# Performance work log

Hardware: AMD Instinct MI355X
Metric: run time of the kernel (lower is better)

## Reference

```python
import jax, jax.numpy as jnp
import numpy as np

N, C, H, W = 4, 256, 64, 64
S = 2          # scale_factor
K = 5          # up_kernel
G = 1          # up_group
CK = 64        # compressed_channels


def conv2d(x, w, b, pad):
    out = jax.lax.conv_general_dilated(
        x, w, window_strides=(1, 1), padding=[(pad, pad), (pad, pad)],
        dimension_numbers=('NCHW', 'OIHW', 'NCHW'))
    return out + b[None, :, None, None]


def pixel_shuffle(x, r):
    n, cr, h, w = x.shape
    c = cr // (r * r)
    return x.reshape(n, c, r, r, h, w).transpose(0, 1, 4, 2, 5, 3).reshape(n, c, h * r, w * r)


def grid_sample_border(img, grid):
    # img [N,C,Hi,Wi], grid [N,Ho,Wo,2] in [-1,1] (x,y); bilinear, border pad, align_corners=True
    n, c, hi, wi = img.shape
    gx = (grid[..., 0] + 1.0) * 0.5 * (wi - 1)
    gy = (grid[..., 1] + 1.0) * 0.5 * (hi - 1)
    gx = jnp.clip(gx, 0.0, wi - 1.0)
    gy = jnp.clip(gy, 0.0, hi - 1.0)
    x0 = jnp.floor(gx).astype(jnp.int32)
    y0 = jnp.floor(gy).astype(jnp.int32)
    x1 = jnp.minimum(x0 + 1, wi - 1)
    y1 = jnp.minimum(y0 + 1, hi - 1)
    wx = (gx - x0)[..., None]
    wy = (gy - y0)[..., None]
    bidx = jnp.arange(n)[:, None, None]
    def gather(yy, xx):
        return img[bidx, :, yy, xx]  # [N,Ho,Wo,C]
    v00 = gather(y0, x0)
    v01 = gather(y0, x1)
    v10 = gather(y1, x0)
    v11 = gather(y1, x1)
    out = (v00 * (1 - wx) * (1 - wy) + v01 * wx * (1 - wy)
           + v10 * (1 - wx) * wy + v11 * wx * wy)
    return out.transpose(0, 3, 1, 2)


def carafe2(features, masks, k, g, up):
    n, c, h, w = features.shape
    cg = c // g
    k2 = k * k
    # masks [N, g*k2, h*up, w*up] -> per-pixel kernels [n,g,h,w,k2,up2]
    m = masks.reshape(n, g, k2, h, up, w, up)
    m = m.transpose(0, 1, 2, 3, 5, 4, 6).reshape(n, g, k2, h, w, up * up)
    kern = m.transpose(0, 1, 3, 4, 2, 5)            # [n,g,h,w,k2,up2]
    f = features.reshape(n, g, cg, h, w)
    p = k // 2
    fp = jnp.pad(f, ((0, 0), (0, 0), (0, 0), (p, p), (p, p)))
    patches = jnp.stack([fp[:, :, :, i:i + h, j:j + w]
                         for i in range(k) for j in range(k)], axis=-1)  # [n,g,cg,h,w,k2]
    xp = patches.transpose(0, 1, 3, 4, 2, 5)        # [n,g,h,w,cg,k2]
    out = jnp.einsum('nghwck,nghwku->nghwcu', xp, kern)  # [n,g,h,w,cg,up2]
    out = out.transpose(0, 1, 4, 2, 3, 5).reshape(n, c * up * up, h, w)
    return pixel_shuffle(out, up)


def setup_inputs() -> dict:
    key = jax.random.key(0)
    ks = jax.random.split(key, 4)
    x = jax.random.normal(ks[0], (N, C, H, W), dtype=jnp.float32)
    w_comp = jax.random.normal(ks[1], (CK, C, 1, 1), dtype=jnp.float32) * 0.05
    b_comp = jnp.zeros((CK,), dtype=jnp.float32)
    w_ker = jax.random.normal(ks[2], (G * K * K, CK, 3, 3), dtype=jnp.float32) * 0.001
    b_ker = jnp.zeros((G * K * K,), dtype=jnp.float32)
    w_off = jax.random.normal(ks[3], (G * 2 * S * S, CK, 3, 3), dtype=jnp.float32) * 0.01
    b_off = jnp.zeros((G * 2 * S * S,), dtype=jnp.float32)
    return {'x': x, 'w_comp': w_comp, 'b_comp': b_comp,
            'w_ker': w_ker, 'b_ker': b_ker, 'w_off': w_off, 'b_off': b_off}


def reference(x, w_comp, b_comp, w_ker, b_ker, w_off, b_off):
    cx = conv2d(x, w_comp, b_comp, 0)               # channel compressor (1x1)
    offset = conv2d(cx, w_off, b_off, 1)            # [N, 2*S*S, H, W]
    mask = conv2d(cx, w_ker, b_ker, 1)              # [N, G*K*K, H, W]
    # kernel_space_normalizer: softmax over the K*K kernel positions
    n, mc, h, w = mask.shape
    mask = jax.nn.softmax(mask.reshape(n, mc // (K * K), K * K, h, w), axis=2)
    mask = mask.reshape(n, mc, h, w)
    # kernel_space_expander
    off = pixel_shuffle(offset, S).transpose(0, 2, 3, 1)  # [N, H*S, W*S, 2]
    off = off * jnp.array([2.0 / (w - 1), 2.0 / (h - 1)], dtype=off.dtype)
    gh = jnp.repeat(jnp.linspace(-1.0, 1.0, h), S)  # [H*S]
    gw = jnp.repeat(jnp.linspace(-1.0, 1.0, w), S)  # [W*S]
    base = jnp.stack(jnp.broadcast_arrays(gw[None, :], gh[:, None]), axis=-1)  # [H*S, W*S, 2]
    grid = base[None] + off
    mask_ = grid_sample_border(mask, grid)          # [N, G*K*K, H*S, W*S]
    return carafe2(x, mask_, K, G, S)
```

## Files before the change

### kernel.cpp

```cpp
#include <hip/hip_runtime.h>
#include <math.h>

#define NB 4
#define C_IN 256
#define CKC 64
#define HWSZ 4096
#define K2 25
#define NOC2 40

#define WS_CX    0
#define WS_OFF   (WS_CX + NB*CKC*HWSZ)
#define WS_MASK  (WS_OFF + NB*8*HWSZ)
#define WS_WT    (WS_MASK + NB*K2*HWSZ)

#define NWT (CKC * 9 * NOC2)
#define NWC (C_IN * CKC)

#define BARRIER_LDS() do { \
    asm volatile("s_waitcnt lgkmcnt(0)" ::: "memory"); \
    __builtin_amdgcn_s_barrier(); \
  } while (0)

__global__ void k_wt(const float* __restrict__ wk, const float* __restrict__ wo,
                     const float* __restrict__ wc,
                     float* __restrict__ wT, float* __restrict__ wcT) {
  int i = blockIdx.x * 256 + threadIdx.x;
  if (i < NWT) {
    int oc = i % NOC2;
    int r = i / NOC2;
    int tap = r % 9, c = r / 9;
    float v = 0.f;
    if (oc < 8)       v = wo[(oc * CKC + c) * 9 + tap];
    else if (oc < 33) v = wk[((oc - 8) * CKC + c) * 9 + tap];
    wT[i] = v;
  } else {
    int j = i - NWT;
    if (j < NWC) {
      int c = j >> 6, ck = j & 63;
      wcT[j] = wc[ck * C_IN + c];
    }
  }
}

__global__ __launch_bounds__(1024) void k_cs(const float* __restrict__ x,
    const float* __restrict__ wcT, const float* __restrict__ bc,
    const float* __restrict__ wT, const float* __restrict__ bk, const float* __restrict__ bo,
    float* __restrict__ offb, float* __restrict__ maskb) {
  __attribute__((aligned(16))) __shared__ float s_mem[15360];
  float* s_tile = s_mem;
  float* s_res  = s_mem;

  int t = threadIdx.x;
  int n = blockIdx.y;
  int tile = blockIdx.x;
  int x0 = (tile & 3) * 16, y0 = (tile >> 2) * 4;
  const float* xn = x + (size_t)n * (C_IN * HWSZ);

  int p = t & 63;
  int w = t >> 6;
  int g = __builtin_amdgcn_readfirstlane(w & 7);
  int ch = __builtin_amdgcn_readfirstlane(w >> 3);

  int srcOff[4];
  unsigned vbits = 0, wbits = 0;
  #pragma unroll
  for (int it = 0; it < 4; it++) {
    int e = t + it * 1024;
    int c = e / 60;
    int rem = e - c * 60;
    int row = rem / 10, pr = rem - row * 10;
    int gy = y0 - 1 + row;
    int gc0 = x0 - 2 + pr * 2;
    bool wr = (e < 3840);
    bool ok = wr & ((unsigned)gy < 64u) & ((unsigned)gc0 < 63u);
    srcOff[it] = ok ? (c * HWSZ + gy * 64 + gc0) : 0;
    vbits |= (ok ? 1u : 0u) << it;
    wbits |= (wr ? 1u : 0u) << it;
  }

  int q1 = p + 60;
  int q1c = (q1 < 120) ? q1 : 119;
  int r0q = p / 20,  c0q = p - r0q * 20;
  int r1q = q1c / 20, c1q = q1c - r1q * 20;
  bool val0 = (c0q >= 1) & (c0q <= 18);
  bool val1 = (q1 < 120) & (c1q >= 1) & (c1q <= 18);
  int toff0 = r0q * 24 + c0q - 1;
  int toff1 = r1q * 24 + c1q - 1;
  float a0[8], a1[8];
  #pragma unroll
  for (int i = 0; i < 8; i++) {
    float b = (ch == 0) ? bc[g * 8 + i] : 0.f;
    a0[i] = b; a1[i] = b;
  }

  float2 rv[4];
  #pragma unroll
  for (int it = 0; it < 4; it++) rv[it] = *(const float2*)(xn + srcOff[it]);

  float* sA = s_mem;
  float* sB = s_mem + 7680;
  #pragma unroll
  for (int it = 0; it < 4; it++)
    if (wbits & (1u << it))
      *(float2*)(&sA[2 * t + it * 2048]) =
          (vbits & (1u << it)) ? rv[it] : make_float2(0.f, 0.f);
  {
    const float* xb = xn + (size_t)64 * HWSZ;
    #pragma unroll
    for (int it = 0; it < 4; it++) rv[it] = *(const float2*)(xb + srcOff[it]);
  }
  BARRIER_LDS();

  for (int k = 0; k < 4; k++) {
    if (k < 3) {
      #pragma unroll
      for (int it = 0; it < 4; it++)
        if (wbits & (1u << it))
          *(float2*)(&sB[2 * t + it * 2048]) =
              (vbits & (1u << it)) ? rv[it] : make_float2(0.f, 0.f);
    }
    if (k < 2) {
      const float* xb = xn + (size_t)(k + 2) * 64 * HWSZ;
      #pragma unroll
      for (int it = 0; it < 4; it++) rv[it] = *(const float2*)(xb + srcOff[it]);
    }
    if ((k >> 1) == ch) {
      const float* wbase = wcT + (k * 64) * 64 + g * 8;
      #pragma unroll 4
      for (int c = 0; c < 64; c++) {
        float v0 = sA[c * 120 + p];
        float v1 = sA[c * 120 + q1c];
        const float* wp = wbase + c * 64;
        #pragma unroll
        for (int i = 0; i < 8; i++) { a0[i] += v0 * wp[i]; a1[i] += v1 * wp[i]; }
      }
    }
    BARRIER_LDS();
    float* tmp = sA; sA = sB; sB = tmp;
  }

  if (ch == 1) {
    if (val0) {
      #pragma unroll
      for (int i = 0; i < 8; i++) s_tile[(g * 8 + i) * 144 + toff0] = a0[i];
    }
    if (val1) {
      #pragma unroll
      for (int i = 0; i < 8; i++) s_tile[(g * 8 + i) * 144 + toff1] = a1[i];
    }
  }
  BARRIER_LDS();
  if (ch == 0) {
    if (val0) {
      #pragma unroll
      for (int i = 0; i < 8; i++) {
        int idx = (g * 8 + i) * 144 + toff0;
        s_tile[idx] = s_tile[idx] + a0[i];
      }
    }
    if (val1) {
      #pragma unroll
      for (int i = 0; i < 8; i++) {
        int idx = (g * 8 + i) * 144 + toff1;
        s_tile[idx] = s_tile[idx] + a1[i];
      }
    }
  }
  BARRIER_LDS();

  int px = p & 15, py = p >> 4;
  float acc[5];
  #pragma unroll
  for (int j = 0; j < 5; j++) acc[j] = 0.f;
  const float* wg = wT + g * 5;
  const float* tl0 = s_tile + py * 24 + px;
  int cb = ch * 32;

#define LOADWIN(dst, cidx)                                   \
  {                                                          \
    const float* tlc = tl0 + (cidx) * 144;                   \
    _Pragma("unroll")                                        \
    for (int tap = 0; tap < 9; tap++) {                      \
      int dy = tap / 3, dx = tap % 3;                        \
      dst[tap] = tlc[dy * 24 + dx];                          \
    }                                                        \
  }
#define FMAWIN(src, cidx)                                    \
  {                                                          \
    const float* wc9 = wg + (cidx) * 9 * NOC2;               \
    _Pragma("unroll")                                        \
    for (int tap = 0; tap < 9; tap++) {                      \
      float v = src[tap];                                    \
      const float* wp = wc9 + tap * NOC2;                    \
      _Pragma("unroll")                                      \
      for (int j = 0; j < 5; j++) acc[j] += v * wp[j];       \
    }                                                        \
  }

  float wa[9], wbuf[9];
  LOADWIN(wa, cb + 0)
  LOADWIN(wbuf, cb + 1)
  #pragma unroll 1
  for (int c = 0; c < 32; c += 2) {
    FMAWIN(wa, cb + c)
    if (c + 2 < 32) LOADWIN(wa, cb + c + 2)
    FMAWIN(wbuf, cb + c + 1)
    if (c + 3 < 32) LOADWIN(wbuf, cb + c + 3)
  }
#undef LOADWIN
#undef FMAWIN

  BARRIER_LDS();
  if (ch == 0) {
    #pragma unroll
    for (int j = 0; j < 5; j++) s_res[(g * 5 + j) * 64 + p] = acc[j];
  }
  BARRIER_LDS();
  if (ch == 1) {
    #pragma unroll
    for (int j = 0; j < 5; j++) s_res[(g * 5 + j) * 64 + p] += acc[j];
  }
  BARRIER_LDS();

  int hw = (y0 + py) * 64 + x0 + px;
  if (ch == 0)
    offb[(n * 8 + g) * HWSZ + hw] = s_res[g * 64 + p] + bo[g];
  if (t < 64) {
    float m[25], mx = -1e30f;
    #pragma unroll
    for (int k = 0; k < 25; k++) { m[k] = s_res[(8 + k) * 64 + p] + bk[k]; mx = fmaxf(mx, m[k]); }
    float s = 0.f;
    #pragma unroll
    for (int k = 0; k < 25; k++) { m[k] = __expf(m[k] - mx); s += m[k]; }
    float inv = 1.f / s;
    #pragma unroll
    for (int k = 0; k < 25; k++) maskb[(n * 25 + k) * HWSZ + hw] = m[k] * inv;
  }
}

__global__ __launch_bounds__(256, 4) void k_carafe(const float* __restrict__ x,
    const float* __restrict__ offb, const float* __restrict__ maskb,
    float* __restrict__ out) {
  __attribute__((aligned(16))) __shared__ float s_patch[32 * 202];
  __attribute__((aligned(16))) __shared__ float s_kern[32 * 25 * 4];
  int t = threadIdx.x;
  int b = blockIdx.x;
  int n = b >> 8;
  int r = b & 255;
  int half = r & 1;
  int wq = (r >> 1) & 3;
  int aa = r >> 3;
  int a = aa + (aa & 16);
  int yout = (a & 15) * 8 + wq * 2 + ((a >> 5) & 1);
  int w0 = wq * 16;
  int cbase = n * C_IN + half * 128;

  int srcOff[13];
  int dstOff[13];
  unsigned vbits = 0;
  unsigned wbits = 0;
  #pragma unroll
  for (int it = 0; it < 13; it++) {
    int e = t + it * 256;
    int c = e / 100;
    int rem = e - c * 100;
    int rg = rem / 10;
    int c2 = rem - rg * 10;
    int row = (rg < 5) ? (a - 2 + rg) : (a + 9 + rg);
    int gc0 = w0 - 2 + c2 * 2;
    bool wr = (e < 3200);
    bool ok = wr & ((unsigned)row < 64u) & ((unsigned)gc0 < 64u);
    srcOff[it] = ok ? (c * HWSZ + row * 64 + gc0) : 0;
    dstOff[it] = wr ? 2 * (e + c) : 0;
    vbits |= (ok ? 1u : 0u) << it;
    wbits |= (wr ? 1u : 0u) << it;
  }

  float2 rv[13];
  {
    const float* xn = x + (size_t)cbase * HWSZ;
    #pragma unroll
    for (int it = 0; it < 13; it++) rv[it] = *(const float2*)(xn + srcOff[it]);
  }

  if (t < 128) {
    int p = t >> 2, u = t & 3;
    int hb = p >> 4, wl = p & 15;
    int h = a + hb * 16;
    int wcol = w0 + wl;
    float ox = offb[(n * 8 + u) * HWSZ + h * 64 + wcol];
    float oy = offb[(n * 8 + 4 + u) * HWSZ + h * 64 + wcol];
    float gx = fminf(fmaxf((float)wcol + ox, 0.f), 63.f);
    float gy = fminf(fmaxf((float)h + oy, 0.f), 63.f);
    float fx0 = floorf(gx), fy0 = floorf(gy);
    int x0 = (int)fx0, y0 = (int)fy0;
    float fx = gx - fx0, fy = gy - fy0;
    int x1 = min(x0 + 1, 63), y1 = min(y0 + 1, 63);
    float w11 = fx * fy;
    float w10 = fy - w11, w01 = fx - w11, w00 = 1.f - fx - fy + w11;
    const float* mb = maskb + n * (K2 * HWSZ);
    int i00 = y0 * 64 + x0, i01 = y0 * 64 + x1;
    int i10 = y1 * 64 + x0, i11 = y1 * 64 + x1;
    #pragma unroll 5
    for (int k = 0; k < 25; k++) {
      const float* mk = mb + k * HWSZ;
      float v = w00 * mk[i00] + w01 * mk[i01] + w10 * mk[i10] + w11 * mk[i11];
      s_kern[(p * 25 + k) * 4 + u] = v;
    }
  }

  int cl = t & 31, g = t >> 5;
  int hb = g >> 2, wl0 = (g & 3) * 4;
  float* s_out = s_patch;

  for (int cc = 0; cc < 4; cc++) {
    BARRIER_LDS();
    #pragma unroll
    for (int it = 0; it < 13; it++) {
      if (wbits & (1u << it)) {
        float2 v = (vbits & (1u << it)) ? rv[it] : make_float2(0.f, 0.f);
        *(float2*)(&s_patch[dstOff[it]]) = v;
      }
    }
    BARRIER_LDS();
    if (cc < 3) {
      const float* xn = x + (size_t)(cbase + (cc + 1) * 32) * HWSZ;
      #pragma unroll
      for (int it = 0; it < 13; it++) rv[it] = *(const float2*)(xn + srcOff[it]);
    }
    float acc[4][4];
    #pragma unroll
    for (int i = 0; i < 4; i++)
      acc[i][0] = acc[i][1] = acc[i][2] = acc[i][3] = 0.f;
    const float* pc = s_patch + cl * 202 + hb * 100 + wl0;
    #pragma unroll
    for (int dy = 0; dy < 5; dy++) {
      float r8[8];
      #pragma unroll
      for (int j = 0; j < 8; j++) r8[j] = pc[dy * 20 + j];
      #pragma unroll
      for (int pr = 0; pr < 4; pr++) {
        const float4* kp = (const float4*)(s_kern + (((g * 4 + pr) * 25) + dy * 5) * 4);
        #pragma unroll
        for (int dx = 0; dx < 5; dx++) {
          float f = r8[pr + dx];
          float4 k4 = kp[dx];
          acc[pr][0] += f * k4.x;
          acc[pr][1] += f * k4.y;
          acc[pr][2] += f * k4.z;
          acc[pr][3] += f * k4.w;
        }
      }
    }
    BARRIER_LDS();
    #pragma unroll
    for (int pr = 0; pr < 4; pr++) {
      int wl = wl0 + pr;
      #pragma unroll
      for (int u = 0; u < 4; u++) {
        int xo = wl * 8 + u * 2 + hb;
        s_out[cl * 130 + xo] = acc[pr][u];
      }
    }
    BARRIER_LDS();
    float* obase = out + ((size_t)(cbase + cc * 32) * 128 + yout) * 128;
    #pragma unroll
    for (int it = 0; it < 4; it++) {
      int q2 = t + it * 256;
      int rowc = q2 >> 5;
      int col4 = q2 & 31;
      const float* sp = s_out + rowc * 130 + col4 * 4;
      float4 v = make_float4(sp[0], sp[1], sp[2], sp[3]);
      *(float4*)(obase + (size_t)rowc * (128 * 128) + col4 * 4) = v;
    }
  }
}

extern "C" void kernel_launch(void* const* d_in, const int* in_sizes, int n_in,
                              void* d_out, int out_size, void* d_ws, size_t ws_size,
                              hipStream_t stream) {
  const float* x      = (const float*)d_in[0];
  const float* w_comp = (const float*)d_in[1];
  const float* b_comp = (const float*)d_in[2];
  const float* w_ker  = (const float*)d_in[3];
  const float* b_ker  = (const float*)d_in[4];
  const float* w_off  = (const float*)d_in[5];
  const float* b_off  = (const float*)d_in[6];
  float* out = (float*)d_out;
  float* ws = (float*)d_ws;
  float* offb  = ws + WS_OFF;
  float* maskb = ws + WS_MASK;
  float* wT    = ws + WS_WT;
  float* wcT   = ws + WS_CX;

  hipLaunchKernelGGL(k_wt, dim3((NWT + NWC + 255) / 256), dim3(256), 0, stream,
                     w_ker, w_off, w_comp, wT, wcT);
  hipLaunchKernelGGL(k_cs, dim3(64, 4), dim3(1024), 0, stream,
                     x, wcT, b_comp, wT, b_ker, b_off, offb, maskb);
  hipLaunchKernelGGL(k_carafe, dim3(1024), dim3(256), 0, stream, x, offb, maskb, out);
}
```

Measured before the change: 172.7 us.

## Halve k_cs spatial tile to 8x4 to double block count

Shrinks the compressor and mask/offset conv tile from 16x4 to 8x4 pixels, so the haloed input tile drops to 6x12 and each thread computes one compressed pixel instead of two. The grid doubles to 128x4 blocks, which should fill more CUs on a device with 256 CUs and cut LDS use per block. In exchange, the 3x3 halo is recomputed more often relative to useful output, and half of each wave sits idle during the 3x3 conv stage.

```diff
diff --git a/kernel.cpp b/kernel.cpp
--- a/kernel.cpp
+++ b/kernel.cpp
@@ -46,14 +46,14 @@
     const float* __restrict__ wcT, const float* __restrict__ bc,
     const float* __restrict__ wT, const float* __restrict__ bk, const float* __restrict__ bo,
     float* __restrict__ offb, float* __restrict__ maskb) {
-  __attribute__((aligned(16))) __shared__ float s_mem[15360];
+  __attribute__((aligned(16))) __shared__ float s_mem[9216];
   float* s_tile = s_mem;
   float* s_res  = s_mem;
 
   int t = threadIdx.x;
   int n = blockIdx.y;
   int tile = blockIdx.x;
-  int x0 = (tile & 3) * 16, y0 = (tile >> 2) * 4;
+  int x0 = (tile & 7) * 8, y0 = (tile >> 3) * 4;
   const float* xn = x + (size_t)n * (C_IN * HWSZ);
 
   int p = t & 63;
@@ -61,128 +61,106 @@
   int g = __builtin_amdgcn_readfirstlane(w & 7);
   int ch = __builtin_amdgcn_readfirstlane(w >> 3);
 
-  int srcOff[4];
+  int srcOff[3];
   unsigned vbits = 0, wbits = 0;
   #pragma unroll
-  for (int it = 0; it < 4; it++) {
+  for (int it = 0; it < 3; it++) {
     int e = t + it * 1024;
-    int c = e / 60;
-    int rem = e - c * 60;
-    int row = rem / 10, pr = rem - row * 10;
+    int c = e / 36;
+    int rem = e - c * 36;
+    int row = rem / 6, pr = rem - row * 6;
     int gy = y0 - 1 + row;
     int gc0 = x0 - 2 + pr * 2;
-    bool wr = (e < 3840);
+    bool wr = (e < 2304);
     bool ok = wr & ((unsigned)gy < 64u) & ((unsigned)gc0 < 63u);
     srcOff[it] = ok ? (c * HWSZ + gy * 64 + gc0) : 0;
     vbits |= (ok ? 1u : 0u) << it;
     wbits |= (wr ? 1u : 0u) << it;
   }
 
-  int q1 = p + 60;
-  int q1c = (q1 < 120) ? q1 : 119;
-  int r0q = p / 20,  c0q = p - r0q * 20;
-  int r1q = q1c / 20, c1q = q1c - r1q * 20;
-  bool val0 = (c0q >= 1) & (c0q <= 18);
-  bool val1 = (q1 < 120) & (c1q >= 1) & (c1q <= 18);
-  int toff0 = r0q * 24 + c0q - 1;
-  int toff1 = r1q * 24 + c1q - 1;
-  float a0[8], a1[8];
-  #pragma unroll
-  for (int i = 0; i < 8; i++) {
-    float b = (ch == 0) ? bc[g * 8 + i] : 0.f;
-    a0[i] = b; a1[i] = b;
-  }
-
-  float2 rv[4];
-  #pragma unroll
-  for (int it = 0; it < 4; it++) rv[it] = *(const float2*)(xn + srcOff[it]);
+  int pos = (p < 60) ? p : 59;
+  int prow = pos / 10, pcol = pos - prow * 10;
+  int paddr = prow * 12 + pcol + 1;
+  bool pval = (p < 60);
+  float a[8];
+  #pragma unroll
+  for (int i = 0; i < 8; i++) a[i] = (ch == 0) ? bc[g * 8 + i] : 0.f;
+
+  float2 rv[3];
+  #pragma unroll
+  for (int it = 0; it < 3; it++) rv[it] = *(const float2*)(xn + srcOff[it]);
 
   float* sA = s_mem;
-  float* sB = s_mem + 7680;
-  #pragma unroll
-  for (int it = 0; it < 4; it++)
+  float* sB = s_mem + 4608;
+  #pragma unroll
+  for (int it = 0; it < 3; it++)
     if (wbits & (1u << it))
-      *(float2*)(&sA[2 * t + it * 2048]) =
+      *(float2*)(&sA[2 * (t + it * 1024)]) =
           (vbits & (1u << it)) ? rv[it] : make_float2(0.f, 0.f);
   {
     const float* xb = xn + (size_t)64 * HWSZ;
     #pragma unroll
-    for (int it = 0; it < 4; it++) rv[it] = *(const float2*)(xb + srcOff[it]);
+    for (int it = 0; it < 3; it++) rv[it] = *(const float2*)(xb + srcOff[it]);
   }
   BARRIER_LDS();
 
   for (int k = 0; k < 4; k++) {
     if (k < 3) {
       #pragma unroll
-      for (int it = 0; it < 4; it++)
+      for (int it = 0; it < 3; it++)
         if (wbits & (1u << it))
-          *(float2*)(&sB[2 * t + it * 2048]) =
+          *(float2*)(&sB[2 * (t + it * 1024)]) =
               (vbits & (1u << it)) ? rv[it] : make_float2(0.f, 0.f);
     }
     if (k < 2) {
       const float* xb = xn + (size_t)(k + 2) * 64 * HWSZ;
       #pragma unroll
-      for (int it = 0; it < 4; it++) rv[it] = *(const float2*)(xb + srcOff[it]);
+      for (int it = 0; it < 3; it++) rv[it] = *(const float2*)(xb + srcOff[it]);
     }
     if ((k >> 1) == ch) {
       const float* wbase = wcT + (k * 64) * 64 + g * 8;
       #pragma unroll 4
       for (int c = 0; c < 64; c++) {
-        float v0 = sA[c * 120 + p];
-        float v1 = sA[c * 120 + q1c];
+        float v = sA[c * 72 + paddr];
         const float* wp = wbase + c * 64;
         #pragma unroll
-        for (int i = 0; i < 8; i++) { a0[i] += v0 * wp[i]; a1[i] += v1 * wp[i]; }
+        for (int i = 0; i < 8; i++) a[i] += v * wp[i];
       }
     }
     BARRIER_LDS();
     float* tmp = sA; sA = sB; sB = tmp;
   }
 
-  if (ch == 1) {
-    if (val0) {
-      #pragma unroll
-      for (int i = 0; i < 8; i++) s_tile[(g * 8 + i) * 144 + toff0] = a0[i];
-    }
-    if (val1) {
-      #pragma unroll
-      for (int i = 0; i < 8; i++) s_tile[(g * 8 + i) * 144 + toff1] = a1[i];
-    }
-  }
-  BARRIER_LDS();
-  if (ch == 0) {
-    if (val0) {
-      #pragma unroll
-      for (int i = 0; i < 8; i++) {
-        int idx = (g * 8 + i) * 144 + toff0;
-        s_tile[idx] = s_tile[idx] + a0[i];
-      }
-    }
-    if (val1) {
-      #pragma unroll
-      for (int i = 0; i < 8; i++) {
-        int idx = (g * 8 + i) * 144 + toff1;
-        s_tile[idx] = s_tile[idx] + a1[i];
-      }
-    }
-  }
-  BARRIER_LDS();
-
-  int px = p & 15, py = p >> 4;
+  if (ch == 1 && pval) {
+    #pragma unroll
+    for (int i = 0; i < 8; i++) s_tile[(g * 8 + i) * 64 + pos] = a[i];
+  }
+  BARRIER_LDS();
+  if (ch == 0 && pval) {
+    #pragma unroll
+    for (int i = 0; i < 8; i++) {
+      int idx = (g * 8 + i) * 64 + pos;
+      s_tile[idx] = s_tile[idx] + a[i];
+    }
+  }
+  BARRIER_LDS();
+
+  int px = p & 7, py = (p >> 3) & 3;
+  bool cact = (p < 32);
   float acc[5];
   #pragma unroll
   for (int j = 0; j < 5; j++) acc[j] = 0.f;
   const float* wg = wT + g * 5;
-  const float* tl0 = s_tile + py * 24 + px;
+  const float* tl0 = s_tile + py * 10 + px;
   int cb = ch * 32;
 
 #define LOADWIN(dst, cidx)                                   \
   {                                                          \
-    const float* tlc = tl0 + (cidx) * 144;                   \
+    const float* tlc = tl0 + (cidx) * 64;                    \
     _Pragma("unroll")                                        \
     for (int tap = 0; tap < 9; tap++) {                      \
       int dy = tap / 3, dx = tap % 3;                        \
-      dst[tap] = tlc[dy * 24 + dx];                          \
+      dst[tap] = tlc[dy * 10 + dx];                          \
     }                                                        \
   }
 #define FMAWIN(src, cidx)                                    \
@@ -197,44 +175,47 @@
     }                                                        \
   }
 
-  float wa[9], wbuf[9];
-  LOADWIN(wa, cb + 0)
-  LOADWIN(wbuf, cb + 1)
-  #pragma unroll 1
-  for (int c = 0; c < 32; c += 2) {
-    FMAWIN(wa, cb + c)
-    if (c + 2 < 32) LOADWIN(wa, cb + c + 2)
-    FMAWIN(wbuf, cb + c + 1)
-    if (c + 3 < 32) LOADWIN(wbuf, cb + c + 3)
+  if (cact) {
+    float wa[9], wbuf[9];
+    LOADWIN(wa, cb + 0)
+    LOADWIN(wbuf, cb + 1)
+    #pragma unroll 1
+    for (int c = 0; c < 32; c += 2) {
+      FMAWIN(wa, cb + c)
+      if (c + 2 < 32) LOADWIN(wa, cb + c + 2)
+      FMAWIN(wbuf, cb + c + 1)
+      if (c + 3 < 32) LOADWIN(wbuf, cb + c + 3)
+    }
   }
 #undef LOADWIN
 #undef FMAWIN
 
   BARRIER_LDS();
-  if (ch == 0) {
-    #pragma unroll
-    for (int j = 0; j < 5; j++) s_res[(g * 5 + j) * 64 + p] = acc[j];
-  }
-  BARRIER_LDS();
-  if (ch == 1) {
-    #pragma unroll
-    for (int j = 0; j < 5; j++) s_res[(g * 5 + j) * 64 + p] += acc[j];
+  if (ch == 0 && cact) {
+    #pragma unroll
+    for (int j = 0; j < 5; j++) s_res[(g * 5 + j) * 32 + p] = acc[j];
+  }
+  BARRIER_LDS();
+  if (ch == 1 && cact) {
+    #pragma unroll
+    for (int j = 0; j < 5; j++) s_res[(g * 5 + j) * 32 + p] += acc[j];
   }
   BARRIER_LDS();
 
   int hw = (y0 + py) * 64 + x0 + px;
-  if (ch == 0)
-    offb[(n * 8 + g) * HWSZ + hw] = s_res[g * 64 + p] + bo[g];
-  if (t < 64) {
+  if (ch == 0 && cact)
+    offb[(n * 8 + g) * HWSZ + hw] = s_res[g * 32 + p] + bo[g];
+  if (t < 32) {
     float m[25], mx = -1e30f;
     #pragma unroll
-    for (int k = 0; k < 25; k++) { m[k] = s_res[(8 + k) * 64 + p] + bk[k]; mx = fmaxf(mx, m[k]); }
+    for (int k = 0; k < 25; k++) { m[k] = s_res[(8 + k) * 32 + t] + bk[k]; mx = fmaxf(mx, m[k]); }
     float s = 0.f;
     #pragma unroll
     for (int k = 0; k < 25; k++) { m[k] = __expf(m[k] - mx); s += m[k]; }
     float inv = 1.f / s;
-    #pragma unroll
-    for (int k = 0; k < 25; k++) maskb[(n * 25 + k) * HWSZ + hw] = m[k] * inv;
+    int hw0 = (y0 + ((t >> 3) & 3)) * 64 + x0 + (t & 7);
+    #pragma unroll
+    for (int k = 0; k < 25; k++) maskb[(n * 25 + k) * HWSZ + hw0] = m[k] * inv;
   }
 }
 
@@ -395,7 +376,7 @@
 
   hipLaunchKernelGGL(k_wt, dim3((NWT + NWC + 255) / 256), dim3(256), 0, stream,
                      w_ker, w_off, w_comp, wT, wcT);
-  hipLaunchKernelGGL(k_cs, dim3(64, 4), dim3(1024), 0, stream,
+  hipLaunchKernelGGL(k_cs, dim3(128, 4), dim3(1024), 0, stream,
                      x, wcT, b_comp, wT, b_ker, b_off, offb, maskb);
   hipLaunchKernelGGL(k_carafe, dim3(1024), dim3(256), 0, stream, x, offb, maskb, out);
 }
```

Measured after the change: 208.6 us. 20.8% more time.
